# Optimization experiments

Measured on AMD Instinct MI355X. Metric: run time of the kernel, lower is better.

The kernel has to match this reference:

```python
import jax, jax.numpy as jnp
import numpy as np

B, N, D = 2048, 128, 32   # samples, features, per-feature embed dim
H = 8                     # num_head
ND = N * D                # flattened width = 4096
U = D * N // H            # per-head units = 512
DH = D // H               # per-head output feature dim = 4


def setup_inputs() -> dict:
    key = jax.random.key(0)
    k_x, k_q, k_k, k_v, k_o = jax.random.split(key, 5)
    scale_w = 0.02  # keep QK^T logits in a sane range for softmax
    x = jax.random.normal(k_x, (B, N, D), dtype=jnp.float32)
    Wq = jax.random.normal(k_q, (H, ND, U), dtype=jnp.float32) * scale_w
    Wk = jax.random.normal(k_k, (H, ND, U), dtype=jnp.float32) * scale_w
    Wv = jax.random.normal(k_v, (H, ND, U), dtype=jnp.float32) * scale_w
    Wo = jax.random.normal(k_o, (D, D), dtype=jnp.float32) * (1.0 / np.sqrt(D))
    return {"x": x, "Wq": Wq, "Wk": Wk, "Wv": Wv, "Wo": Wo}


def reference(x, Wq, Wk, Wv, Wo):
    b, n, d = x.shape
    scale = d ** (-0.5)          # note: original scales by feature dim d, not head dim
    xf = x.reshape(b, n * d)     # (b, nd); the leading 1 axis in TF is vacuous
    # Batched per-head projections (collapses the Python head loop into one GEMM each)
    q = jnp.einsum('bf,hfu->hbu', xf, Wq)   # (H, b, U)
    k = jnp.einsum('bf,hfu->hbu', xf, Wk)   # (H, b, U)
    v = jnp.einsum('bf,hfu->hbu', xf, Wv)   # (H, b, U)
    scores = jax.nn.softmax(jnp.einsum('hbu,hcu->hbc', q, k) * scale, axis=-1)  # (H, b, b)
    av = jnp.einsum('hbc,hcu->hbu', scores, v)              # (H, b, U)
    # per-head reshape (b, U) -> (b, n, d/H), then concat heads along last dim
    av = av.reshape(H, b, n, d // H)                         # (H, b, n, dh)
    concat = jnp.transpose(av, (1, 2, 0, 3)).reshape(b, n, d)  # (b, n, d)
    return concat @ Wo  # dropout rate is 0 -> identity
```

## Files before the change

### kernel.cpp

```cpp
#include <hip/hip_runtime.h>
#include <stdint.h>
#include <math.h>

typedef short    s16x8 __attribute__((ext_vector_type(8)));
typedef float    f32x4 __attribute__((ext_vector_type(4)));
typedef uint32_t u32x4 __attribute__((ext_vector_type(4)));
typedef unsigned short u16x4 __attribute__((ext_vector_type(4)));

__device__ __forceinline__ uint16_t f2bf(float f) {
  union { float f; uint32_t u; } v; v.f = f;
  uint32_t r = v.u + 0x7fffu + ((v.u >> 16) & 1u);
  return (uint16_t)(r >> 16);
}
__device__ __forceinline__ float bf2f(uint16_t h) {
  union { uint32_t u; float f; } v; v.u = ((uint32_t)h) << 16;
  return v.f;
}

__device__ __forceinline__ void gld16(const void* g, void* l) {
  __builtin_amdgcn_global_load_lds(
      (const __attribute__((address_space(1))) void*)g,
      (__attribute__((address_space(3))) void*)l, 16, 0, 0);
}

__global__ __launch_bounds__(256) void cvt_x(const float* __restrict__ x,
                                             uint16_t* __restrict__ xf,
                                             float* __restrict__ rs) {
  if (blockIdx.x < 64) rs[blockIdx.x * 256 + threadIdx.x] = 0.f;
  size_t i = ((size_t)blockIdx.x * 256 + threadIdx.x) * 4;
  f32x4 v = *(const f32x4*)(x + i);
  u16x4 o = { f2bf(v.x), f2bf(v.y), f2bf(v.z), f2bf(v.w) };
  *(u16x4*)(xf + i) = o;
}

__global__ __launch_bounds__(256) void wtrans(const float* __restrict__ W0,
                                              const float* __restrict__ W1,
                                              const float* __restrict__ W2,
                                              uint16_t* __restrict__ Wt) {
  const int z = blockIdx.z;
  const float* W = (z < 8 ? W0 : (z < 16 ? W1 : W2)) + (size_t)(z & 7) * (4096 * 512);
  const int f0 = blockIdx.x * 32, u0 = blockIdx.y * 32;
  __shared__ float t[32][33];
  const int tid = threadIdx.x;
  {
    const int fi = tid >> 3, uu = (tid & 7) * 4;
    f32x4 v = *(const f32x4*)(W + (size_t)(f0 + fi) * 512 + u0 + uu);
    t[fi][uu] = v.x; t[fi][uu + 1] = v.y; t[fi][uu + 2] = v.z; t[fi][uu + 3] = v.w;
  }
  __syncthreads();
  {
    const int ui = tid >> 3, ff = (tid & 7) * 4;
    u16x4 o = { f2bf(t[ff][ui]), f2bf(t[ff + 1][ui]),
                f2bf(t[ff + 2][ui]), f2bf(t[ff + 3][ui]) };
    *(u16x4*)&Wt[((size_t)z * 512 + u0 + ui) * 4096 + f0 + ff] = o;
  }
}

template <int MODE>
__global__ __launch_bounds__(256, 4) void gemm_bt(
    const uint16_t* __restrict__ A, size_t sAz,
    const uint16_t* __restrict__ B, size_t sBz,
    void* __restrict__ C0, void* __restrict__ C1,
    int K, float scale, float* __restrict__ rs) {
  const int tid = threadIdx.x;
  const int wave = tid >> 6, lane = tid & 63;
  const int quad = lane >> 4, l16 = lane & 15;
  const int wrow = (wave >> 1) * 64, wcol = (wave & 1) * 64;
  const int m0 = blockIdx.y * 128, n0 = blockIdx.x * 128;
  const int z = blockIdx.z;
  A += (size_t)z * sAz;
  B += (size_t)z * sBz;

  __shared__ __align__(16) uint16_t lA[128 * 64];
  __shared__ __align__(16) uint16_t lB[128 * 64];

  f32x4 acc[4][4];
#pragma unroll
  for (int i = 0; i < 4; i++)
#pragma unroll
    for (int j = 0; j < 4; j++) acc[i][j] = f32x4{0.f, 0.f, 0.f, 0.f};

  const int lrow = lane >> 3;
  const int cs = ((lane & 7) ^ (lrow & 7)) * 8;
  const int rs0 = wave * 8;
  const uint16_t* gA = A + (size_t)(m0 + rs0 + lrow) * K + cs;
  const uint16_t* gB = B + (size_t)(n0 + rs0 + lrow) * K + cs;
  const size_t row32 = (size_t)32 * K;
  uint16_t* sA = &lA[rs0 * 64];
  uint16_t* sB = &lB[rs0 * 64];

  for (int k0 = 0; k0 < K; k0 += 64) {
    __syncthreads();
#pragma unroll
    for (int g = 0; g < 4; g++) {
      gld16(gA + g * row32, sA + g * 2048);
      gld16(gB + g * row32, sB + g * 2048);
    }
    gA += 64; gB += 64;
    __syncthreads();
#pragma unroll
    for (int h = 0; h < 2; h++) {
      s16x8 af[4], bfr[4];
      const int fsw = (((h * 4 + quad) ^ (l16 & 7)) * 8);
#pragma unroll
      for (int i = 0; i < 4; i++)
        af[i] = *(const s16x8*)&lA[(wrow + i * 16 + l16) * 64 + fsw];
#pragma unroll
      for (int j = 0; j < 4; j++)
        bfr[j] = *(const s16x8*)&lB[(wcol + j * 16 + l16) * 64 + fsw];
#pragma unroll
      for (int i = 0; i < 4; i++)
#pragma unroll
        for (int j = 0; j < 4; j++)
          acc[i][j] = __builtin_amdgcn_mfma_f32_16x16x32_bf16(af[i], bfr[j], acc[i][j], 0, 0, 0);
    }
  }

  const int mb = m0 + wrow + quad * 4;
  const int nb = n0 + wcol + l16;
  if (MODE == 4) {
    if (z < 16) {
      uint16_t* C = (uint16_t*)C0 + ((size_t)z << 20);
#pragma unroll
      for (int i = 0; i < 4; i++)
#pragma unroll
        for (int j = 0; j < 4; j++)
#pragma unroll
          for (int r = 0; r < 4; r++)
            C[(size_t)(mb + i * 16 + r) * 512 + (nb + j * 16)] = f2bf(acc[i][j][r]);
    } else {
      uint16_t* C = (uint16_t*)C1 + ((size_t)(z - 16) << 20);
#pragma unroll
      for (int i = 0; i < 4; i++)
#pragma unroll
        for (int j = 0; j < 4; j++) {
          u16x4 o = { f2bf(acc[i][j][0]), f2bf(acc[i][j][1]),
                      f2bf(acc[i][j][2]), f2bf(acc[i][j][3]) };
          *(u16x4*)&((uint16_t*)C)[(size_t)(nb + j * 16) * 2048 + (mb + i * 16)] = o;
        }
    }
  } else if (MODE == 2) {
    uint16_t* C = (uint16_t*)C0 + ((size_t)z << 22);
    float* rz = rs + (z << 11);
    float si[4][4];
#pragma unroll
    for (int i = 0; i < 4; i++)
#pragma unroll
      for (int r = 0; r < 4; r++) si[i][r] = 0.f;
#pragma unroll
    for (int i = 0; i < 4; i++)
#pragma unroll
      for (int j = 0; j < 4; j++)
#pragma unroll
        for (int r = 0; r < 4; r++) {
          float e = exp2f(fmaf(acc[i][j][r], scale, -43.2808512f));
          uint16_t hb = f2bf(e);
          C[(size_t)(mb + i * 16 + r) * 2048 + (nb + j * 16)] = hb;
          si[i][r] += bf2f(hb);
        }
#pragma unroll
    for (int i = 0; i < 4; i++)
#pragma unroll
      for (int r = 0; r < 4; r++) {
        float s = si[i][r];
        s += __shfl_xor(s, 1);
        s += __shfl_xor(s, 2);
        s += __shfl_xor(s, 4);
        s += __shfl_xor(s, 8);
        si[i][r] = s;
      }
    if (l16 == 0) {
#pragma unroll
      for (int i = 0; i < 4; i++)
#pragma unroll
        for (int r = 0; r < 4; r++)
          atomicAdd(&rz[mb + i * 16 + r], si[i][r]);
    }
  } else {
    float* C = (float*)C0 + ((size_t)z << 20);
    const float* rz = rs + (z << 11);
#pragma unroll
    for (int i = 0; i < 4; i++)
#pragma unroll
      for (int r = 0; r < 4; r++) {
        float w = 1.0f / rz[mb + i * 16 + r];
#pragma unroll
        for (int j = 0; j < 4; j++)
          C[(size_t)(mb + i * 16 + r) * 512 + (nb + j * 16)] = acc[i][j][r] * w;
      }
  }
}

__global__ __launch_bounds__(256) void out_proj(const float* __restrict__ av,
                                                const float* __restrict__ Wo,
                                                float* __restrict__ out) {
  __shared__ float lw[1024];
  const int tid = threadIdx.x;
#pragma unroll
  for (int i = 0; i < 4; i++) lw[tid + i * 256] = Wo[tid + i * 256];
  __syncthreads();
  const int p = blockIdx.x * 256 + tid;
  const int b = p >> 7, n = p & 127;
  float c[32];
#pragma unroll
  for (int h = 0; h < 8; h++) {
    f32x4 v = *(const f32x4*)(av + ((size_t)h * 2048 + b) * 512 + n * 4);
    c[h * 4] = v.x; c[h * 4 + 1] = v.y; c[h * 4 + 2] = v.z; c[h * 4 + 3] = v.w;
  }
  float o[32];
#pragma unroll
  for (int d = 0; d < 32; d++) o[d] = 0.f;
#pragma unroll
  for (int j = 0; j < 32; j++) {
    float cj = c[j];
#pragma unroll
    for (int d = 0; d < 32; d++) o[d] = fmaf(cj, lw[j * 32 + d], o[d]);
  }
  float* dst = out + (size_t)p * 32;
#pragma unroll
  for (int i = 0; i < 8; i++) {
    f32x4 v = { o[i * 4], o[i * 4 + 1], o[i * 4 + 2], o[i * 4 + 3] };
    *(f32x4*)(dst + i * 4) = v;
  }
}

extern "C" void kernel_launch(void* const* d_in, const int* in_sizes, int n_in,
                              void* d_out, int out_size, void* d_ws, size_t ws_size,
                              hipStream_t stream) {
  const float* x  = (const float*)d_in[0];
  const float* Wq = (const float*)d_in[1];
  const float* Wk = (const float*)d_in[2];
  const float* Wv = (const float*)d_in[3];
  const float* Wo = (const float*)d_in[4];
  float* out = (float*)d_out;

  uint8_t* ws = (uint8_t*)d_ws;
  uint16_t* Wt = (uint16_t*)(ws);
  uint16_t* P  = (uint16_t*)(ws);
  float*    av = (float*)(ws + 67108864);
  uint16_t* xf = (uint16_t*)(ws + 100663296);
  uint16_t* q  = (uint16_t*)(ws + 117440512);
  uint16_t* vt = (uint16_t*)(ws + 150994944);
  float*    rs = (float*)(ws + 167772160);

  const size_t WtH = (size_t)512 * 4096;
  const float scale2 = 0.17677669529663687f * 1.4426950408889634f;

  cvt_x<<<8192, 256, 0, stream>>>(x, xf, rs);
  wtrans<<<dim3(128, 16, 24), 256, 0, stream>>>(Wq, Wk, Wv, Wt);

  gemm_bt<4><<<dim3(4, 16, 24), 256, 0, stream>>>(
      xf, 0, Wt, WtH, q, vt, 4096, 0.f, nullptr);

  gemm_bt<2><<<dim3(16, 16, 8), 256, 0, stream>>>(
      q, (size_t)2048 * 512, q + (size_t)8 * 2048 * 512, (size_t)2048 * 512,
      P, nullptr, 512, scale2, rs);

  gemm_bt<3><<<dim3(4, 16, 8), 256, 0, stream>>>(
      P, (size_t)2048 * 2048, vt, (size_t)512 * 2048,
      av, nullptr, 2048, 0.f, rs);

  out_proj<<<1024, 256, 0, stream>>>(av, Wo, out);
}
```

Before: 572.1 us.

## Switch GEMMs to 32x32 MFMA, split-K the PV GEMM, widen weight transpose

Replaces the 16x16x32 bf16 MFMA tiles with 32x32x16 tiles (2x2 per wave), which need fewer LDS fragment reads per FLOP. The P·V GEMM is split into two K halves written to separate buffers and summed in out_proj, doubling its grid to raise occupancy at the cost of extra fp32 traffic. The weight transpose kernel now handles 64x32 tiles with 8-wide bf16 stores. The softmax row-sum reduction is adapted to the new accumulator layout.

New measurement: 617.3 us. 7.9% more time.

```diff
diff --git a/kernel.cpp b/kernel.cpp
--- a/kernel.cpp
+++ b/kernel.cpp
@@ -2,10 +2,12 @@
 #include <stdint.h>
 #include <math.h>
 
-typedef short    s16x8 __attribute__((ext_vector_type(8)));
-typedef float    f32x4 __attribute__((ext_vector_type(4)));
-typedef uint32_t u32x4 __attribute__((ext_vector_type(4)));
+typedef short    s16x8  __attribute__((ext_vector_type(8)));
+typedef float    f32x4  __attribute__((ext_vector_type(4)));
+typedef float    f32x16 __attribute__((ext_vector_type(16)));
+typedef uint32_t u32x4  __attribute__((ext_vector_type(4)));
 typedef unsigned short u16x4 __attribute__((ext_vector_type(4)));
+typedef unsigned short u16x8 __attribute__((ext_vector_type(8)));
 
 __device__ __forceinline__ uint16_t f2bf(float f) {
   union { float f; uint32_t u; } v; v.f = f;
@@ -39,20 +41,24 @@
                                               uint16_t* __restrict__ Wt) {
   const int z = blockIdx.z;
   const float* W = (z < 8 ? W0 : (z < 16 ? W1 : W2)) + (size_t)(z & 7) * (4096 * 512);
-  const int f0 = blockIdx.x * 32, u0 = blockIdx.y * 32;
-  __shared__ float t[32][33];
+  const int f0 = blockIdx.x * 64, u0 = blockIdx.y * 32;
+  __shared__ float t[64][33];
   const int tid = threadIdx.x;
   {
-    const int fi = tid >> 3, uu = (tid & 7) * 4;
-    f32x4 v = *(const f32x4*)(W + (size_t)(f0 + fi) * 512 + u0 + uu);
-    t[fi][uu] = v.x; t[fi][uu + 1] = v.y; t[fi][uu + 2] = v.z; t[fi][uu + 3] = v.w;
+    const int fi = tid >> 2, uu = (tid & 3) * 8;
+    const float* src = W + (size_t)(f0 + fi) * 512 + u0 + uu;
+    f32x4 v0 = *(const f32x4*)src;
+    f32x4 v1 = *(const f32x4*)(src + 4);
+    t[fi][uu] = v0.x; t[fi][uu + 1] = v0.y; t[fi][uu + 2] = v0.z; t[fi][uu + 3] = v0.w;
+    t[fi][uu + 4] = v1.x; t[fi][uu + 5] = v1.y; t[fi][uu + 6] = v1.z; t[fi][uu + 7] = v1.w;
   }
   __syncthreads();
   {
-    const int ui = tid >> 3, ff = (tid & 7) * 4;
-    u16x4 o = { f2bf(t[ff][ui]), f2bf(t[ff + 1][ui]),
-                f2bf(t[ff + 2][ui]), f2bf(t[ff + 3][ui]) };
-    *(u16x4*)&Wt[((size_t)z * 512 + u0 + ui) * 4096 + f0 + ff] = o;
+    const int uo = tid >> 3, fo = (tid & 7) * 8;
+    u16x8 o = { f2bf(t[fo][uo]),     f2bf(t[fo + 1][uo]), f2bf(t[fo + 2][uo]),
+                f2bf(t[fo + 3][uo]), f2bf(t[fo + 4][uo]), f2bf(t[fo + 5][uo]),
+                f2bf(t[fo + 6][uo]), f2bf(t[fo + 7][uo]) };
+    *(u16x8*)&Wt[((size_t)z * 512 + u0 + uo) * 4096 + f0 + fo] = o;
   }
 }
 
@@ -64,21 +70,24 @@
     int K, float scale, float* __restrict__ rs) {
   const int tid = threadIdx.x;
   const int wave = tid >> 6, lane = tid & 63;
-  const int quad = lane >> 4, l16 = lane & 15;
+  const int l31 = lane & 31, h = lane >> 5;
   const int wrow = (wave >> 1) * 64, wcol = (wave & 1) * 64;
   const int m0 = blockIdx.y * 128, n0 = blockIdx.x * 128;
-  const int z = blockIdx.z;
-  A += (size_t)z * sAz;
-  B += (size_t)z * sBz;
+  int z = blockIdx.z, kh = 0, Kloop = K;
+  if (MODE == 3) { kh = z >> 3; z &= 7; Kloop = K >> 1; }
+  A += (size_t)z * sAz + (size_t)kh * Kloop;
+  B += (size_t)z * sBz + (size_t)kh * Kloop;
 
   __shared__ __align__(16) uint16_t lA[128 * 64];
   __shared__ __align__(16) uint16_t lB[128 * 64];
 
-  f32x4 acc[4][4];
-#pragma unroll
-  for (int i = 0; i < 4; i++)
-#pragma unroll
-    for (int j = 0; j < 4; j++) acc[i][j] = f32x4{0.f, 0.f, 0.f, 0.f};
+  f32x16 acc[2][2];
+#pragma unroll
+  for (int i = 0; i < 2; i++)
+#pragma unroll
+    for (int j = 0; j < 2; j++)
+#pragma unroll
+      for (int r = 0; r < 16; r++) acc[i][j][r] = 0.f;
 
   const int lrow = lane >> 3;
   const int cs = ((lane & 7) ^ (lrow & 7)) * 8;
@@ -89,7 +98,7 @@
   uint16_t* sA = &lA[rs0 * 64];
   uint16_t* sB = &lB[rs0 * 64];
 
-  for (int k0 = 0; k0 < K; k0 += 64) {
+  for (int k0 = 0; k0 < Kloop; k0 += 64) {
     __syncthreads();
 #pragma unroll
     for (int g = 0; g < 4; g++) {
@@ -99,99 +108,115 @@
     gA += 64; gB += 64;
     __syncthreads();
 #pragma unroll
-    for (int h = 0; h < 2; h++) {
-      s16x8 af[4], bfr[4];
-      const int fsw = (((h * 4 + quad) ^ (l16 & 7)) * 8);
-#pragma unroll
-      for (int i = 0; i < 4; i++)
-        af[i] = *(const s16x8*)&lA[(wrow + i * 16 + l16) * 64 + fsw];
-#pragma unroll
-      for (int j = 0; j < 4; j++)
-        bfr[j] = *(const s16x8*)&lB[(wcol + j * 16 + l16) * 64 + fsw];
-#pragma unroll
-      for (int i = 0; i < 4; i++)
-#pragma unroll
-        for (int j = 0; j < 4; j++)
-          acc[i][j] = __builtin_amdgcn_mfma_f32_16x16x32_bf16(af[i], bfr[j], acc[i][j], 0, 0, 0);
-    }
-  }
-
-  const int mb = m0 + wrow + quad * 4;
-  const int nb = n0 + wcol + l16;
+    for (int s = 0; s < 4; s++) {
+      const int fsw = (((s * 2 + h) ^ (lane & 7)) * 8);
+      s16x8 af[2], bfr[2];
+#pragma unroll
+      for (int i = 0; i < 2; i++)
+        af[i] = *(const s16x8*)&lA[(wrow + i * 32 + l31) * 64 + fsw];
+#pragma unroll
+      for (int j = 0; j < 2; j++)
+        bfr[j] = *(const s16x8*)&lB[(wcol + j * 32 + l31) * 64 + fsw];
+#pragma unroll
+      for (int i = 0; i < 2; i++)
+#pragma unroll
+        for (int j = 0; j < 2; j++)
+          acc[i][j] = __builtin_amdgcn_mfma_f32_32x32x16_bf16(af[i], bfr[j], acc[i][j], 0, 0, 0);
+    }
+  }
+
   if (MODE == 4) {
     if (z < 16) {
       uint16_t* C = (uint16_t*)C0 + ((size_t)z << 20);
 #pragma unroll
-      for (int i = 0; i < 4; i++)
-#pragma unroll
-        for (int j = 0; j < 4; j++)
-#pragma unroll
-          for (int r = 0; r < 4; r++)
-            C[(size_t)(mb + i * 16 + r) * 512 + (nb + j * 16)] = f2bf(acc[i][j][r]);
+      for (int i = 0; i < 2; i++) {
+        const int rb = m0 + wrow + i * 32 + 4 * h;
+#pragma unroll
+        for (int j = 0; j < 2; j++) {
+          const int col = n0 + wcol + j * 32 + l31;
+#pragma unroll
+          for (int g = 0; g < 4; g++)
+#pragma unroll
+            for (int r = 0; r < 4; r++)
+              C[(size_t)(rb + 8 * g + r) * 512 + col] = f2bf(acc[i][j][g * 4 + r]);
+        }
+      }
     } else {
       uint16_t* C = (uint16_t*)C1 + ((size_t)(z - 16) << 20);
 #pragma unroll
-      for (int i = 0; i < 4; i++)
-#pragma unroll
-        for (int j = 0; j < 4; j++) {
-          u16x4 o = { f2bf(acc[i][j][0]), f2bf(acc[i][j][1]),
-                      f2bf(acc[i][j][2]), f2bf(acc[i][j][3]) };
-          *(u16x4*)&((uint16_t*)C)[(size_t)(nb + j * 16) * 2048 + (mb + i * 16)] = o;
-        }
+      for (int i = 0; i < 2; i++) {
+        const int rb = m0 + wrow + i * 32 + 4 * h;
+#pragma unroll
+        for (int j = 0; j < 2; j++) {
+          const int col = n0 + wcol + j * 32 + l31;
+#pragma unroll
+          for (int g = 0; g < 4; g++) {
+            u16x4 o = { f2bf(acc[i][j][g * 4]),     f2bf(acc[i][j][g * 4 + 1]),
+                        f2bf(acc[i][j][g * 4 + 2]), f2bf(acc[i][j][g * 4 + 3]) };
+            *(u16x4*)&C[(size_t)col * 2048 + rb + 8 * g] = o;
+          }
+        }
+      }
     }
   } else if (MODE == 2) {
     uint16_t* C = (uint16_t*)C0 + ((size_t)z << 22);
     float* rz = rs + (z << 11);
-    float si[4][4];
-#pragma unroll
-    for (int i = 0; i < 4; i++)
-#pragma unroll
-      for (int r = 0; r < 4; r++) si[i][r] = 0.f;
-#pragma unroll
-    for (int i = 0; i < 4; i++)
-#pragma unroll
-      for (int j = 0; j < 4; j++)
+#pragma unroll
+    for (int i = 0; i < 2; i++) {
+      const int rb = m0 + wrow + i * 32 + 4 * h;
+#pragma unroll
+      for (int j = 0; j < 2; j++) {
+        const int col = n0 + wcol + j * 32 + l31;
+#pragma unroll
+        for (int g = 0; g < 4; g++)
+#pragma unroll
+          for (int r = 0; r < 4; r++) {
+            float e = exp2f(fmaf(acc[i][j][g * 4 + r], scale, -43.2808512f));
+            uint16_t hb = f2bf(e);
+            C[(size_t)(rb + 8 * g + r) * 2048 + col] = hb;
+            acc[i][j][g * 4 + r] = bf2f(hb);
+          }
+      }
+    }
+#pragma unroll
+    for (int i = 0; i < 2; i++) {
+      const int rb = m0 + wrow + i * 32 + 4 * h;
+#pragma unroll
+      for (int g = 0; g < 4; g++)
 #pragma unroll
         for (int r = 0; r < 4; r++) {
-          float e = exp2f(fmaf(acc[i][j][r], scale, -43.2808512f));
-          uint16_t hb = f2bf(e);
-          C[(size_t)(mb + i * 16 + r) * 2048 + (nb + j * 16)] = hb;
-          si[i][r] += bf2f(hb);
-        }
-#pragma unroll
-    for (int i = 0; i < 4; i++)
-#pragma unroll
-      for (int r = 0; r < 4; r++) {
-        float s = si[i][r];
-        s += __shfl_xor(s, 1);
-        s += __shfl_xor(s, 2);
-        s += __shfl_xor(s, 4);
-        s += __shfl_xor(s, 8);
-        si[i][r] = s;
-      }
-    if (l16 == 0) {
-#pragma unroll
-      for (int i = 0; i < 4; i++)
-#pragma unroll
-        for (int r = 0; r < 4; r++)
-          atomicAdd(&rz[mb + i * 16 + r], si[i][r]);
+          float s = acc[i][0][g * 4 + r] + acc[i][1][g * 4 + r];
+          s += __shfl_xor(s, 1);
+          s += __shfl_xor(s, 2);
+          s += __shfl_xor(s, 4);
+          s += __shfl_xor(s, 8);
+          s += __shfl_xor(s, 16);
+          if (l31 == 0) atomicAdd(&rz[rb + 8 * g + r], s);
+        }
     }
   } else {
-    float* C = (float*)C0 + ((size_t)z << 20);
+    float* C = (float*)(kh ? C1 : C0) + ((size_t)z << 20);
     const float* rz = rs + (z << 11);
 #pragma unroll
-    for (int i = 0; i < 4; i++)
-#pragma unroll
-      for (int r = 0; r < 4; r++) {
-        float w = 1.0f / rz[mb + i * 16 + r];
-#pragma unroll
-        for (int j = 0; j < 4; j++)
-          C[(size_t)(mb + i * 16 + r) * 512 + (nb + j * 16)] = acc[i][j][r] * w;
-      }
-  }
-}
-
-__global__ __launch_bounds__(256) void out_proj(const float* __restrict__ av,
+    for (int i = 0; i < 2; i++) {
+      const int rb = m0 + wrow + i * 32 + 4 * h;
+#pragma unroll
+      for (int g = 0; g < 4; g++) {
+        f32x4 rv = *(const f32x4*)&rz[rb + 8 * g];
+#pragma unroll
+        for (int j = 0; j < 2; j++) {
+          const int col = n0 + wcol + j * 32 + l31;
+#pragma unroll
+          for (int r = 0; r < 4; r++)
+            C[(size_t)(rb + 8 * g + r) * 512 + col] = acc[i][j][g * 4 + r] / rv[r];
+        }
+      }
+    }
+  }
+}
+
+__global__ __launch_bounds__(256) void out_proj(const float* __restrict__ av0,
+                                                const float* __restrict__ av1,
                                                 const float* __restrict__ Wo,
                                                 float* __restrict__ out) {
   __shared__ float lw[1024];
@@ -203,9 +228,12 @@
   const int b = p >> 7, n = p & 127;
   float c[32];
 #pragma unroll
-  for (int h = 0; h < 8; h++) {
-    f32x4 v = *(const f32x4*)(av + ((size_t)h * 2048 + b) * 512 + n * 4);
-    c[h * 4] = v.x; c[h * 4 + 1] = v.y; c[h * 4 + 2] = v.z; c[h * 4 + 3] = v.w;
+  for (int hh = 0; hh < 8; hh++) {
+    size_t idx = ((size_t)hh * 2048 + b) * 512 + n * 4;
+    f32x4 v = *(const f32x4*)(av0 + idx);
+    f32x4 w = *(const f32x4*)(av1 + idx);
+    c[hh * 4] = v.x + w.x; c[hh * 4 + 1] = v.y + w.y;
+    c[hh * 4 + 2] = v.z + w.z; c[hh * 4 + 3] = v.w + w.w;
   }
   float o[32];
 #pragma unroll
@@ -235,19 +263,20 @@
   float* out = (float*)d_out;
 
   uint8_t* ws = (uint8_t*)d_ws;
-  uint16_t* Wt = (uint16_t*)(ws);
-  uint16_t* P  = (uint16_t*)(ws);
-  float*    av = (float*)(ws + 67108864);
-  uint16_t* xf = (uint16_t*)(ws + 100663296);
-  uint16_t* q  = (uint16_t*)(ws + 117440512);
-  uint16_t* vt = (uint16_t*)(ws + 150994944);
-  float*    rs = (float*)(ws + 167772160);
+  uint16_t* Wt  = (uint16_t*)(ws);
+  uint16_t* P   = (uint16_t*)(ws);
+  float*    av0 = (float*)(ws + 67108864);
+  uint16_t* xf  = (uint16_t*)(ws + 100663296);
+  uint16_t* q   = (uint16_t*)(ws + 117440512);
+  float*    av1 = (float*)(ws + 117440512);
+  uint16_t* vt  = (uint16_t*)(ws + 150994944);
+  float*    rs  = (float*)(ws + 167772160);
 
   const size_t WtH = (size_t)512 * 4096;
   const float scale2 = 0.17677669529663687f * 1.4426950408889634f;
 
   cvt_x<<<8192, 256, 0, stream>>>(x, xf, rs);
-  wtrans<<<dim3(128, 16, 24), 256, 0, stream>>>(Wq, Wk, Wv, Wt);
+  wtrans<<<dim3(64, 16, 24), 256, 0, stream>>>(Wq, Wk, Wv, Wt);
 
   gemm_bt<4><<<dim3(4, 16, 24), 256, 0, stream>>>(
       xf, 0, Wt, WtH, q, vt, 4096, 0.f, nullptr);
@@ -256,9 +285,9 @@
       q, (size_t)2048 * 512, q + (size_t)8 * 2048 * 512, (size_t)2048 * 512,
       P, nullptr, 512, scale2, rs);
 
-  gemm_bt<3><<<dim3(4, 16, 8), 256, 0, stream>>>(
+  gemm_bt<3><<<dim3(4, 16, 16), 256, 0, stream>>>(
       P, (size_t)2048 * 2048, vt, (size_t)512 * 2048,
-      av, nullptr, 2048, 0.f, rs);
-
-  out_proj<<<1024, 256, 0, stream>>>(av, Wo, out);
-}
+      av0, av1, 2048, 0.f, rs);
+
+  out_proj<<<1024, 256, 0, stream>>>(av0, av1, Wo, out);
+}
```
